# Performance work log

Hardware: AMD Instinct MI355X
Metric: run time of the kernel (lower is better)

The kernel has to match this reference:

```python
import jax, jax.numpy as jnp
import numpy as np

N, F, P, O, E = 20000, 8, 12, 32, 320000


def setup_inputs() -> dict:
    key = jax.random.key(0)
    ks = jax.random.split(key, 18)
    g = lambda k, shape: (jax.random.normal(k, shape, jnp.float32) * 0.1)
    x = jax.random.normal(ks[0], (N, F, P), jnp.float32)
    edge_index = jax.random.randint(ks[1], (2, E), 0, N, dtype=jnp.int32)
    return {
        "x": x,
        "edge_index": edge_index,
        # GCNConv weights/biases for update (z), reset (r), candidate (h) gates
        "Wz": g(ks[2], (F, O)), "bz": g(ks[3], (O,)),
        "Wr": g(ks[4], (F, O)), "br": g(ks[5], (O,)),
        "Wh": g(ks[6], (F, O)), "bh": g(ks[7], (O,)),
        # GRU linear layers (torch.nn.Linear: y = x @ W.T + b), in=2*O, out=O
        "lz_w": g(ks[8], (O, 2 * O)), "lz_b": g(ks[9], (O,)),
        "lr_w": g(ks[10], (O, 2 * O)), "lr_b": g(ks[11], (O,)),
        "lh_w": g(ks[12], (O, 2 * O)), "lh_b": g(ks[13], (O,)),
        # temporal attention logits over periods
        "att": g(ks[14], (P,)),
        # final Linear(32 -> window_size)
        "out_w": g(ks[15], (P, O)), "out_b": g(ks[16], (P,)),
    }


def reference(x, edge_index, Wz, bz, Wr, br, Wh, bh,
              lz_w, lz_b, lr_w, lr_b, lh_w, lh_b, att, out_w, out_b):
    n = x.shape[0]
    # gcn_norm with self-loops: norm_e = d^-1/2[src] * d^-1/2[dst]
    loop = jnp.arange(n, dtype=edge_index.dtype)
    src = jnp.concatenate([edge_index[0], loop])
    dst = jnp.concatenate([edge_index[1], loop])
    deg = jax.ops.segment_sum(jnp.ones(src.shape[0], x.dtype), dst, num_segments=n)
    dinv = jnp.where(deg > 0, deg ** -0.5, 0.0)
    norm = dinv[src] * dinv[dst]  # [E+n]

    def gcn(xp, W, b):
        # xp: [n, P, F] -> [n, P, O]; GCNConv: D^-1/2 (A+I) D^-1/2 (X W) + b
        h = jnp.einsum('npf,fo->npo', xp, W)
        msg = h[src] * norm[:, None, None]  # [E+n, P, O]
        return jax.ops.segment_sum(msg, dst, num_segments=n) + b

    xp = jnp.transpose(x, (0, 2, 1))  # [n, P, F]
    # A3TGCN does NOT carry H across periods (H stays initial zeros), so all
    # periods are independent GRU steps from H = 0 and can be batched.
    H = jnp.zeros(xp.shape[:2] + (O,), x.dtype)
    Z = jax.nn.sigmoid(jnp.concatenate([gcn(xp, Wz, bz), H], -1) @ lz_w.T + lz_b)
    R = jax.nn.sigmoid(jnp.concatenate([gcn(xp, Wr, br), H], -1) @ lr_w.T + lr_b)
    Ht = jnp.tanh(jnp.concatenate([gcn(xp, Wh, bh), H * R], -1) @ lh_w.T + lh_b)
    Hp = Z * H + (1.0 - Z) * Ht  # [n, P, O]
    probs = jax.nn.softmax(att)
    Hacc = jnp.einsum('npo,p->no', Hp, probs)  # attention-weighted sum
    return jax.nn.relu(Hacc) @ out_w.T + out_b  # [n, window_size]
```

## Files before the change

kernel.cpp:

```cpp
#include <hip/hip_runtime.h>
#include <math.h>

#define FP 96
#define SLOT 64
#define NPB 8
#define GBLK 128
#define PBLK 256
#define POISON ((int)0xAAAAAAAA)

__device__ __forceinline__ unsigned f2bf_bits(float f) {
    unsigned u = __float_as_uint(f);
    return (u + 0x7fffu + ((u >> 16) & 1u)) >> 16;
}
__device__ __forceinline__ float bf_lo(unsigned u) { return __uint_as_float(u << 16); }
__device__ __forceinline__ float bf_hi(unsigned u) { return __uint_as_float(u & 0xffff0000u); }

__device__ __forceinline__ int cnt_decode(int v) {
    return ((unsigned)v >= 0xAA000000u) ? v - POISON : v;
}

__global__ void k_hist_fold(const int* __restrict__ ei, int E,
                            int* __restrict__ cnt, int* __restrict__ bucket,
                            const float* __restrict__ Wz, const float* __restrict__ bz,
                            const float* __restrict__ Wh, const float* __restrict__ bh,
                            const float* __restrict__ lz_w, const float* __restrict__ lz_b,
                            const float* __restrict__ lh_w, const float* __restrict__ lh_b,
                            const float* __restrict__ att, const float* __restrict__ out_w,
                            const float* __restrict__ out_b, float* __restrict__ cst) {
    int b = blockIdx.x, t = threadIdx.x;
    if (b == gridDim.x - 1) {
        int f = t >> 5, o = t & 31;
        float sz = 0.f, sh = 0.f;
        for (int j = 0; j < 32; ++j) {
            sz += Wz[f * 32 + j] * lz_w[o * 64 + j];
            sh += Wh[f * 32 + j] * lh_w[o * 64 + j];
        }
        cst[t]       = sz;
        cst[256 + t] = sh;
        if (t < 32) {
            float a = lz_b[t], c = lh_b[t];
            for (int j = 0; j < 32; ++j) {
                a += bz[j] * lz_w[t * 64 + j];
                c += bh[j] * lh_w[t * 64 + j];
            }
            cst[512 + t] = a;
            cst[544 + t] = c;
        }
        if (t < 12) {
            float m = -1e30f;
            for (int p = 0; p < 12; ++p) m = fmaxf(m, att[p]);
            float s = 0.f;
            for (int p = 0; p < 12; ++p) s += expf(att[p] - m);
            cst[576 + t] = expf(att[t] - m) / s;
        }
        for (int i = t; i < 384; i += PBLK)
            cst[588 + (i & 31) * 12 + (i >> 5)] = out_w[i];
        if (t < 12) cst[972 + t] = out_b[t];
        return;
    }
    int e2 = b * PBLK + t;
    int e = e2 << 1;
    if (e >= E) return;
    if (e + 1 < E) {
        int2 s2 = ((const int2*)ei)[e2];
        int2 d2 = ((const int2*)(ei + E))[e2];
        int o0 = atomicAdd(cnt + d2.x, 1);
        int o1 = atomicAdd(cnt + d2.y, 1);
        int p0 = cnt_decode(o0), p1 = cnt_decode(o1);
        if (p0 < SLOT) bucket[(size_t)d2.x * SLOT + p0] = s2.x;
        if (p1 < SLOT) bucket[(size_t)d2.y * SLOT + p1] = s2.y;
    } else {
        int src = ei[e], dst = ei[E + e];
        int old = atomicAdd(cnt + dst, 1);
        int pos = cnt_decode(old);
        if (pos < SLOT) bucket[(size_t)dst * SLOT + pos] = src;
    }
}

__global__ void k_convert(const float* __restrict__ x, const int* __restrict__ cnt,
                          unsigned* __restrict__ xb, int N) {
    int i = blockIdx.x * blockDim.x + threadIdx.x;
    if (i >= (N + 1) * 12) return;
    int n = i / 12;
    if (n == N) {
        ((uint4*)xb)[i] = make_uint4(0u, 0u, 0u, 0u);
        return;
    }
    int deg = cnt_decode(cnt[n]);
    float w = rsqrtf((float)(deg + 1));
    const float4* x4 = (const float4*)x;
    float4 a = x4[i * 2], c = x4[i * 2 + 1];
    uint4 r;
    r.x = f2bf_bits(w * a.x) | (f2bf_bits(w * a.y) << 16);
    r.y = f2bf_bits(w * a.z) | (f2bf_bits(w * a.w) << 16);
    r.z = f2bf_bits(w * c.x) | (f2bf_bits(w * c.y) << 16);
    r.w = f2bf_bits(w * c.z) | (f2bf_bits(w * c.w) << 16);
    ((uint4*)xb)[i] = r;
}

__device__ __forceinline__ void load_batch(uint4* P, const uint4* __restrict__ xrow,
                                           const int* list, int k) {
#pragma unroll
    for (int u = 0; u < 8; ++u) P[u] = xrow[list[u] * 12 + k];
}
__device__ __forceinline__ void acc_batch(float* acc, const uint4* C) {
    acc[0] += ((bf_lo(C[0].x) + bf_lo(C[1].x)) + (bf_lo(C[2].x) + bf_lo(C[3].x)))
            + ((bf_lo(C[4].x) + bf_lo(C[5].x)) + (bf_lo(C[6].x) + bf_lo(C[7].x)));
    acc[1] += ((bf_hi(C[0].x) + bf_hi(C[1].x)) + (bf_hi(C[2].x) + bf_hi(C[3].x)))
            + ((bf_hi(C[4].x) + bf_hi(C[5].x)) + (bf_hi(C[6].x) + bf_hi(C[7].x)));
    acc[2] += ((bf_lo(C[0].y) + bf_lo(C[1].y)) + (bf_lo(C[2].y) + bf_lo(C[3].y)))
            + ((bf_lo(C[4].y) + bf_lo(C[5].y)) + (bf_lo(C[6].y) + bf_lo(C[7].y)));
    acc[3] += ((bf_hi(C[0].y) + bf_hi(C[1].y)) + (bf_hi(C[2].y) + bf_hi(C[3].y)))
            + ((bf_hi(C[4].y) + bf_hi(C[5].y)) + (bf_hi(C[6].y) + bf_hi(C[7].y)));
    acc[4] += ((bf_lo(C[0].z) + bf_lo(C[1].z)) + (bf_lo(C[2].z) + bf_lo(C[3].z)))
            + ((bf_lo(C[4].z) + bf_lo(C[5].z)) + (bf_lo(C[6].z) + bf_lo(C[7].z)));
    acc[5] += ((bf_hi(C[0].z) + bf_hi(C[1].z)) + (bf_hi(C[2].z) + bf_hi(C[3].z)))
            + ((bf_hi(C[4].z) + bf_hi(C[5].z)) + (bf_hi(C[6].z) + bf_hi(C[7].z)));
    acc[6] += ((bf_lo(C[0].w) + bf_lo(C[1].w)) + (bf_lo(C[2].w) + bf_lo(C[3].w)))
            + ((bf_lo(C[4].w) + bf_lo(C[5].w)) + (bf_lo(C[6].w) + bf_lo(C[7].w)));
    acc[7] += ((bf_hi(C[0].w) + bf_hi(C[1].w)) + (bf_hi(C[2].w) + bf_hi(C[3].w)))
            + ((bf_hi(C[4].w) + bf_hi(C[5].w)) + (bf_hi(C[6].w) + bf_hi(C[7].w)));
}

__global__ void __launch_bounds__(GBLK, 4)
k_gather_gates(const unsigned* __restrict__ xb, const int* __restrict__ cnt,
               const int* __restrict__ bucket, const float* __restrict__ cst,
               float* __restrict__ out, int N) {
    __shared__ float sy[NPB][FP + 4];
    __shared__ float shr[NPB][32];
    __shared__ float scst[984];
    __shared__ int   sbuck[NPB][72];
    __shared__ int   sdeg[NPB];
    int t = threadIdx.x;
    int n0 = blockIdx.x * NPB;
    const uint4* xrow = (const uint4*)xb;

    int nl = 0, k = 0, n = N;
    uint4 self = make_uint4(0u, 0u, 0u, 0u);
    if (t < NPB * 12) {
        nl = t / 12; k = t - nl * 12; n = n0 + nl;
        if (n < N) self = xrow[n * 12 + k];
    }
    if (t < NPB) sdeg[t] = (n0 + t < N) ? cnt_decode(cnt[n0 + t]) : 0;
    {
        int nd = t >> 4, q = t & 15, nn = n0 + nd;
        if (nn < N) *(int4*)&sbuck[nd][q * 4] =
            ((const int4*)(bucket + (size_t)nn * SLOT))[q];
    }
    for (int i = t; i < 984; i += GBLK) scst[i] = cst[i];
    __syncthreads();
    if (t < NPB * 8) {
        int nnl = t >> 3, q = t & 7;
        int d = min(sdeg[nnl], SLOT);
        int degp = (d + 7) & ~7; if (degp < 8) degp = 8;
        int pos = d + q;
        if (pos < degp) sbuck[nnl][pos] = N;
    }
    __syncthreads();

    if (t < NPB * 12 && n < N) {
        int c = sdeg[nl];
        int d = min(c, SLOT);
        int degp = (d + 7) & ~7; if (degp < 8) degp = 8;
        int nb = degp >> 3;
        const int* list = sbuck[nl];
        float acc[8] = {bf_lo(self.x), bf_hi(self.x), bf_lo(self.y), bf_hi(self.y),
                        bf_lo(self.z), bf_hi(self.z), bf_lo(self.w), bf_hi(self.w)};
        uint4 A[8], C[8];
        load_batch(A, xrow, list, k);
        for (int i = 0; i < nb; ++i) {
#pragma unroll
            for (int u = 0; u < 8; ++u) C[u] = A[u];
            if (i + 1 < nb) load_batch(A, xrow, list + (i + 1) * 8, k);
            acc_batch(acc, C);
        }
        float di = rsqrtf((float)(c + 1));
#pragma unroll
        for (int i = 0; i < 8; ++i) sy[nl][k * 8 + i] = di * acc[i];
    }
    __syncthreads();

    int o = t & 31;
#pragma unroll
    for (int it = 0; it < 2; ++it) {
        int local = (t >> 5) + it * 4, nn = n0 + local;
        if (nn < N) {
            float cz = scst[512 + o], ch = scst[544 + o];
            float hacc = 0.f;
#pragma unroll
            for (int p = 0; p < 12; ++p) {
                float az = cz, ah = ch;
#pragma unroll
                for (int f = 0; f < 8; ++f) {
                    float xf = sy[local][f * 12 + p];
                    az += xf * scst[f * 32 + o];
                    ah += xf * scst[256 + f * 32 + o];
                }
                float ez = __expf(-az);
                float Z  = __builtin_amdgcn_rcpf(1.f + ez);
                float eh = __expf(ah + ah);
                float Ht = 1.f - 2.f * __builtin_amdgcn_rcpf(eh + 1.f);
                hacc += scst[576 + p] * (1.f - Z) * Ht;
            }
            shr[local][o] = fmaxf(hacc, 0.f);
        }
    }
    __syncthreads();
#pragma unroll
    for (int it = 0; it < 2; ++it) {
        int local = (t >> 5) + it * 4, nn = n0 + local;
        if (nn < N && o < 12) {
            float s = scst[972 + o];
#pragma unroll
            for (int j2 = 0; j2 < 32; ++j2)
                s += shr[local][j2] * scst[588 + j2 * 12 + o];
            out[(size_t)nn * 12 + o] = s;
        }
    }
}

extern "C" void kernel_launch(void* const* d_in, const int* in_sizes, int n_in,
                              void* d_out, int out_size, void* d_ws, size_t ws_size,
                              hipStream_t stream) {
    const float* x    = (const float*)d_in[0];
    const int*   ei   = (const int*)d_in[1];
    const float* Wz   = (const float*)d_in[2];
    const float* bz   = (const float*)d_in[3];
    const float* Wh   = (const float*)d_in[6];
    const float* bh   = (const float*)d_in[7];
    const float* lz_w = (const float*)d_in[8];
    const float* lz_b = (const float*)d_in[9];
    const float* lh_w = (const float*)d_in[12];
    const float* lh_b = (const float*)d_in[13];
    const float* att  = (const float*)d_in[14];
    const float* ow   = (const float*)d_in[15];
    const float* ob   = (const float*)d_in[16];
    float* out = (float*)d_out;

    int N = in_sizes[0] / FP;
    int E = in_sizes[1] / 2;

    int*      cnt    = (int*)d_ws;
    int*      bucket = cnt + (N + 1);
    unsigned* xb     = (unsigned*)(bucket + (size_t)N * SLOT);
    float*    cst    = (float*)(xb + (size_t)(N + 1) * 48);

    int EB = (E + PBLK * 2 - 1) / (PBLK * 2);
    k_hist_fold<<<EB + 1, PBLK, 0, stream>>>(ei, E, cnt, bucket, Wz, bz, Wh, bh,
                                             lz_w, lz_b, lh_w, lh_b, att, ow, ob, cst);
    k_convert  <<<((N + 1) * 12 + PBLK - 1) / PBLK, PBLK, 0, stream>>>(x, cnt, xb, N);
    k_gather_gates<<<(N + NPB - 1) / NPB, GBLK, 0, stream>>>(xb, cnt, bucket, cst, out, N);
}
```

Measured before the change: 131.2 us.

## Merge histogram and bf16 conversion into one launch, apply source norm in gather

Folds the edge-histogram/bucket kernel, the x-to-bf16 conversion kernel and the constant-folding block into a single launch. This is possible because conversion no longer pre-scales x by the source-degree factor, which would require the histogram to finish first. Instead, the gather loop loads each neighbour's count alongside its features and applies the rsqrt weight with FMAs. This removes a kernel launch and a serialization point, at the cost of an extra scattered load per neighbour in the gather.

```diff
diff --git a/kernel.cpp b/kernel.cpp
--- a/kernel.cpp
+++ b/kernel.cpp
@@ -19,16 +19,56 @@
     return ((unsigned)v >= 0xAA000000u) ? v - POISON : v;
 }
 
-__global__ void k_hist_fold(const int* __restrict__ ei, int E,
-                            int* __restrict__ cnt, int* __restrict__ bucket,
-                            const float* __restrict__ Wz, const float* __restrict__ bz,
-                            const float* __restrict__ Wh, const float* __restrict__ bh,
-                            const float* __restrict__ lz_w, const float* __restrict__ lz_b,
-                            const float* __restrict__ lh_w, const float* __restrict__ lh_b,
-                            const float* __restrict__ att, const float* __restrict__ out_w,
-                            const float* __restrict__ out_b, float* __restrict__ cst) {
+__global__ void k_prep(const float* __restrict__ x, const int* __restrict__ ei,
+                       const float* __restrict__ Wz, const float* __restrict__ bz,
+                       const float* __restrict__ Wh, const float* __restrict__ bh,
+                       const float* __restrict__ lz_w, const float* __restrict__ lz_b,
+                       const float* __restrict__ lh_w, const float* __restrict__ lh_b,
+                       const float* __restrict__ att, const float* __restrict__ out_w,
+                       const float* __restrict__ out_b,
+                       int* __restrict__ cnt, int* __restrict__ bucket,
+                       unsigned* __restrict__ xb, float* __restrict__ cst,
+                       int N, int E, int EB, int CB) {
     int b = blockIdx.x, t = threadIdx.x;
-    if (b == gridDim.x - 1) {
+    if (b < EB) {
+        int e2 = b * PBLK + t;
+        int e = e2 << 1;
+        if (e >= E) return;
+        if (e + 1 < E) {
+            int2 s2 = ((const int2*)ei)[e2];
+            int2 d2 = ((const int2*)(ei + E))[e2];
+            int o0 = atomicAdd(cnt + d2.x, 1);
+            int o1 = atomicAdd(cnt + d2.y, 1);
+            int p0 = cnt_decode(o0), p1 = cnt_decode(o1);
+            if (p0 < SLOT) bucket[(size_t)d2.x * SLOT + p0] = s2.x;
+            if (p1 < SLOT) bucket[(size_t)d2.y * SLOT + p1] = s2.y;
+        } else {
+            int src = ei[e], dst = ei[E + e];
+            int old = atomicAdd(cnt + dst, 1);
+            int pos = cnt_decode(old);
+            if (pos < SLOT) bucket[(size_t)dst * SLOT + pos] = src;
+        }
+        return;
+    }
+    if (b < EB + CB) {
+        int i = (b - EB) * PBLK + t;
+        if (i >= (N + 1) * 12) return;
+        int n = i / 12;
+        if (n == N) {
+            ((uint4*)xb)[i] = make_uint4(0u, 0u, 0u, 0u);
+            return;
+        }
+        const float4* x4 = (const float4*)x;
+        float4 a = x4[i * 2], c = x4[i * 2 + 1];
+        uint4 r;
+        r.x = f2bf_bits(a.x) | (f2bf_bits(a.y) << 16);
+        r.y = f2bf_bits(a.z) | (f2bf_bits(a.w) << 16);
+        r.z = f2bf_bits(c.x) | (f2bf_bits(c.y) << 16);
+        r.w = f2bf_bits(c.z) | (f2bf_bits(c.w) << 16);
+        ((uint4*)xb)[i] = r;
+        return;
+    }
+    {
         int f = t >> 5, o = t & 31;
         float sz = 0.f, sh = 0.f;
         for (int j = 0; j < 32; ++j) {
@@ -56,70 +96,32 @@
         for (int i = t; i < 384; i += PBLK)
             cst[588 + (i & 31) * 12 + (i >> 5)] = out_w[i];
         if (t < 12) cst[972 + t] = out_b[t];
-        return;
-    }
-    int e2 = b * PBLK + t;
-    int e = e2 << 1;
-    if (e >= E) return;
-    if (e + 1 < E) {
-        int2 s2 = ((const int2*)ei)[e2];
-        int2 d2 = ((const int2*)(ei + E))[e2];
-        int o0 = atomicAdd(cnt + d2.x, 1);
-        int o1 = atomicAdd(cnt + d2.y, 1);
-        int p0 = cnt_decode(o0), p1 = cnt_decode(o1);
-        if (p0 < SLOT) bucket[(size_t)d2.x * SLOT + p0] = s2.x;
-        if (p1 < SLOT) bucket[(size_t)d2.y * SLOT + p1] = s2.y;
-    } else {
-        int src = ei[e], dst = ei[E + e];
-        int old = atomicAdd(cnt + dst, 1);
-        int pos = cnt_decode(old);
-        if (pos < SLOT) bucket[(size_t)dst * SLOT + pos] = src;
-    }
-}
-
-__global__ void k_convert(const float* __restrict__ x, const int* __restrict__ cnt,
-                          unsigned* __restrict__ xb, int N) {
-    int i = blockIdx.x * blockDim.x + threadIdx.x;
-    if (i >= (N + 1) * 12) return;
-    int n = i / 12;
-    if (n == N) {
-        ((uint4*)xb)[i] = make_uint4(0u, 0u, 0u, 0u);
-        return;
-    }
-    int deg = cnt_decode(cnt[n]);
-    float w = rsqrtf((float)(deg + 1));
-    const float4* x4 = (const float4*)x;
-    float4 a = x4[i * 2], c = x4[i * 2 + 1];
-    uint4 r;
-    r.x = f2bf_bits(w * a.x) | (f2bf_bits(w * a.y) << 16);
-    r.y = f2bf_bits(w * a.z) | (f2bf_bits(w * a.w) << 16);
-    r.z = f2bf_bits(w * c.x) | (f2bf_bits(w * c.y) << 16);
-    r.w = f2bf_bits(w * c.z) | (f2bf_bits(w * c.w) << 16);
-    ((uint4*)xb)[i] = r;
-}
-
-__device__ __forceinline__ void load_batch(uint4* P, const uint4* __restrict__ xrow,
-                                           const int* list, int k) {
-#pragma unroll
-    for (int u = 0; u < 8; ++u) P[u] = xrow[list[u] * 12 + k];
-}
-__device__ __forceinline__ void acc_batch(float* acc, const uint4* C) {
-    acc[0] += ((bf_lo(C[0].x) + bf_lo(C[1].x)) + (bf_lo(C[2].x) + bf_lo(C[3].x)))
-            + ((bf_lo(C[4].x) + bf_lo(C[5].x)) + (bf_lo(C[6].x) + bf_lo(C[7].x)));
-    acc[1] += ((bf_hi(C[0].x) + bf_hi(C[1].x)) + (bf_hi(C[2].x) + bf_hi(C[3].x)))
-            + ((bf_hi(C[4].x) + bf_hi(C[5].x)) + (bf_hi(C[6].x) + bf_hi(C[7].x)));
-    acc[2] += ((bf_lo(C[0].y) + bf_lo(C[1].y)) + (bf_lo(C[2].y) + bf_lo(C[3].y)))
-            + ((bf_lo(C[4].y) + bf_lo(C[5].y)) + (bf_lo(C[6].y) + bf_lo(C[7].y)));
-    acc[3] += ((bf_hi(C[0].y) + bf_hi(C[1].y)) + (bf_hi(C[2].y) + bf_hi(C[3].y)))
-            + ((bf_hi(C[4].y) + bf_hi(C[5].y)) + (bf_hi(C[6].y) + bf_hi(C[7].y)));
-    acc[4] += ((bf_lo(C[0].z) + bf_lo(C[1].z)) + (bf_lo(C[2].z) + bf_lo(C[3].z)))
-            + ((bf_lo(C[4].z) + bf_lo(C[5].z)) + (bf_lo(C[6].z) + bf_lo(C[7].z)));
-    acc[5] += ((bf_hi(C[0].z) + bf_hi(C[1].z)) + (bf_hi(C[2].z) + bf_hi(C[3].z)))
-            + ((bf_hi(C[4].z) + bf_hi(C[5].z)) + (bf_hi(C[6].z) + bf_hi(C[7].z)));
-    acc[6] += ((bf_lo(C[0].w) + bf_lo(C[1].w)) + (bf_lo(C[2].w) + bf_lo(C[3].w)))
-            + ((bf_lo(C[4].w) + bf_lo(C[5].w)) + (bf_lo(C[6].w) + bf_lo(C[7].w)));
-    acc[7] += ((bf_hi(C[0].w) + bf_hi(C[1].w)) + (bf_hi(C[2].w) + bf_hi(C[3].w)))
-            + ((bf_hi(C[4].w) + bf_hi(C[5].w)) + (bf_hi(C[6].w) + bf_hi(C[7].w)));
+    }
+}
+
+__device__ __forceinline__ void load_batch_w(uint4* P, int* CR,
+                                             const uint4* __restrict__ xrow,
+                                             const int* __restrict__ cnt,
+                                             const int* list, int k) {
+#pragma unroll
+    for (int u = 0; u < 8; ++u) {
+        int idx = list[u];
+        P[u]  = xrow[idx * 12 + k];
+        CR[u] = cnt[idx];
+    }
+}
+__device__ __forceinline__ void facc_batch(float* acc, const uint4* C, const float* w) {
+#pragma unroll
+    for (int u = 0; u < 8; ++u) {
+        acc[0] += w[u] * bf_lo(C[u].x);
+        acc[1] += w[u] * bf_hi(C[u].x);
+        acc[2] += w[u] * bf_lo(C[u].y);
+        acc[3] += w[u] * bf_hi(C[u].y);
+        acc[4] += w[u] * bf_lo(C[u].z);
+        acc[5] += w[u] * bf_hi(C[u].z);
+        acc[6] += w[u] * bf_lo(C[u].w);
+        acc[7] += w[u] * bf_hi(C[u].w);
+    }
 }
 
 __global__ void __launch_bounds__(GBLK, 4)
@@ -164,17 +166,24 @@
         int degp = (d + 7) & ~7; if (degp < 8) degp = 8;
         int nb = degp >> 3;
         const int* list = sbuck[nl];
-        float acc[8] = {bf_lo(self.x), bf_hi(self.x), bf_lo(self.y), bf_hi(self.y),
-                        bf_lo(self.z), bf_hi(self.z), bf_lo(self.w), bf_hi(self.w)};
-        uint4 A[8], C[8];
-        load_batch(A, xrow, list, k);
+        float di = rsqrtf((float)(c + 1));
+        float acc[8] = {di * bf_lo(self.x), di * bf_hi(self.x),
+                        di * bf_lo(self.y), di * bf_hi(self.y),
+                        di * bf_lo(self.z), di * bf_hi(self.z),
+                        di * bf_lo(self.w), di * bf_hi(self.w)};
+        uint4 A[8], Cb[8];
+        int   crA[8];
+        float w[8];
+        load_batch_w(A, crA, xrow, cnt, list, k);
         for (int i = 0; i < nb; ++i) {
 #pragma unroll
-            for (int u = 0; u < 8; ++u) C[u] = A[u];
-            if (i + 1 < nb) load_batch(A, xrow, list + (i + 1) * 8, k);
-            acc_batch(acc, C);
-        }
-        float di = rsqrtf((float)(c + 1));
+            for (int u = 0; u < 8; ++u) Cb[u] = A[u];
+#pragma unroll
+            for (int u = 0; u < 8; ++u)
+                w[u] = rsqrtf((float)(cnt_decode(crA[u]) + 1));
+            if (i + 1 < nb) load_batch_w(A, crA, xrow, cnt, list + (i + 1) * 8, k);
+            facc_batch(acc, Cb, w);
+        }
 #pragma unroll
         for (int i = 0; i < 8; ++i) sy[nl][k * 8 + i] = di * acc[i];
     }
@@ -246,8 +255,9 @@
     float*    cst    = (float*)(xb + (size_t)(N + 1) * 48);
 
     int EB = (E + PBLK * 2 - 1) / (PBLK * 2);
-    k_hist_fold<<<EB + 1, PBLK, 0, stream>>>(ei, E, cnt, bucket, Wz, bz, Wh, bh,
-                                             lz_w, lz_b, lh_w, lh_b, att, ow, ob, cst);
-    k_convert  <<<((N + 1) * 12 + PBLK - 1) / PBLK, PBLK, 0, stream>>>(x, cnt, xb, N);
+    int CB = ((N + 1) * 12 + PBLK - 1) / PBLK;
+    k_prep<<<EB + CB + 1, PBLK, 0, stream>>>(x, ei, Wz, bz, Wh, bh,
+                                             lz_w, lz_b, lh_w, lh_b, att, ow, ob,
+                                             cnt, bucket, xb, cst, N, E, EB, CB);
     k_gather_gates<<<(N + NPB - 1) / NPB, GBLK, 0, stream>>>(xb, cnt, bucket, cst, out, N);
 }
```

Result: slower. 139.2 us (+6.1%).
